# Optimization experiments

Hardware: AMD Instinct MI355X
Metric: run time of the kernel (lower is better)

The kernel has to match this reference:

```python
import jax, jax.numpy as jnp
import numpy as np

WSIZE = (12, 12)
NUM_HEADS = 12
HEAD_DIM = 64


def _rel_idx(ws):
    wh, ww = ws
    num_dist = (2 * wh - 1) * (2 * ww - 1) + 3
    coords = np.stack(np.meshgrid(np.arange(wh), np.arange(ww), indexing='ij'))
    coords = coords.reshape(2, -1)                       # [2, wh*ww]
    rel = (coords[:, :, None] - coords[:, None, :]).transpose(1, 2, 0)
    rel[:, :, 0] += wh - 1
    rel[:, :, 1] += ww - 1
    rel[:, :, 0] *= 2 * ww - 1
    idx = np.zeros((wh * ww + 1,) * 2, dtype=np.int32)
    idx[1:, 1:] = rel.sum(-1)
    idx[0, 0:] = num_dist - 3
    idx[0:, 0] = num_dist - 2
    idx[0, 0] = num_dist - 1
    return idx.flatten()                                  # [(wh*ww+1)**2]

REL_IDX = jnp.asarray(_rel_idx(WSIZE))


def setup_inputs() -> dict:
    key = jax.random.key(0)
    ks = jax.random.split(key, 8)
    B, S, D = 1024, WSIZE[0] * WSIZE[1] + 1, NUM_HEADS * HEAD_DIM
    num_dist = (2 * WSIZE[0] - 1) * (2 * WSIZE[1] - 1) + 3
    return {
        'x': jax.random.normal(ks[0], (B, S, D), jnp.float32),
        'attn_mask': jax.random.normal(ks[1], (B, 1, S, S), jnp.float32),
        'Wq': jax.random.normal(ks[2], (D, D), jnp.float32) * 0.02,
        'bq': jnp.zeros((D,), jnp.float32),
        'Wk': jax.random.normal(ks[3], (D, D), jnp.float32) * 0.02,
        'Wv': jax.random.normal(ks[4], (D, D), jnp.float32) * 0.02,
        'bv': jnp.zeros((D,), jnp.float32),
        'rel_bias_tbl': jax.random.normal(ks[5], (num_dist, NUM_HEADS), jnp.float32) * 0.02,
    }


def reference(x, attn_mask, Wq, bq, Wk, Wv, bv, rel_bias_tbl):
    B, S, _ = x.shape
    H, D = NUM_HEADS, HEAD_DIM

    def heads(e):  # [B,S,H*D] -> [B,H,S,D]
        return e.reshape(B, S, H, D).transpose(0, 2, 1, 3)

    q = heads(x @ Wq + bq)
    k = heads(x @ Wk)            # key has no bias
    v = heads(x @ Wv + bv)

    scores = jnp.einsum('bhqd,bhkd->bhqk', q, k) / np.sqrt(D).astype(x.dtype)
    scores = scores + attn_mask
    # relative position bias: gather [S*S, H] -> [S,S,H] -> [1,H,S,S]
    rel_bias = rel_bias_tbl[REL_IDX].reshape(S, S, H).transpose(2, 0, 1)[None]
    scores = scores + rel_bias

    probs = jax.nn.softmax(scores, axis=-1)
    ctx = jnp.einsum('bhqk,bhkd->bhqd', probs, v)          # [B,H,S,D]
    return ctx.transpose(0, 2, 1, 3).reshape(B, S, H * D)
```

## Files before the change

kernel.cpp:

```cpp
#include <hip/hip_runtime.h>
#include <hip/hip_bf16.h>

typedef __bf16 bf16x8 __attribute__((ext_vector_type(8)));
typedef float f32x4 __attribute__((ext_vector_type(4)));
typedef float f32x4u __attribute__((ext_vector_type(4), aligned(4)));

#define NH 12
#define HD 64
#define SEQ 145
#define SP 160
#define DMODEL 768
#define NTOT 2304
#define BDIM 1024
#define RBS 148

__device__ __forceinline__ ushort f2bf(float f) {
  union { float f; uint u; } a; a.f = f;
  uint u = a.u;
  return (ushort)((u + 0x7FFFu + ((u >> 16) & 1u)) >> 16);
}

__device__ __forceinline__ int relidx(int qi, int ki) {
  if (ki == 0) return (qi == 0) ? 531 : 530;
  if (qi == 0) return 529;
  int q = qi - 1, k = ki - 1;
  int qh = q / 12, qw = q - qh * 12;
  int kh = k / 12, kw = k - kh * 12;
  return (qh - kh + 11) * 23 + (qw - kw + 11);
}

__device__ __forceinline__ void gload_lds16(const ushort* g, ushort* l) {
  __builtin_amdgcn_global_load_lds(
      (const __attribute__((address_space(1))) void*)g,
      (__attribute__((address_space(3))) void*)l, 16, 0, 0);
}

#define VMCNT(n) do { asm volatile("s_waitcnt vmcnt(" #n ")" ::: "memory"); \
                      __builtin_amdgcn_sched_barrier(0); } while (0)

__global__ void prep_w(const float* __restrict__ Wq, const float* __restrict__ Wk,
                       const float* __restrict__ Wv, ushort* __restrict__ Wt) {
  int i = blockIdx.x * 256 + threadIdx.x;
  if (i >= NTOT * DMODEL) return;
  int n = i / DMODEL, k = i - n * DMODEL;
  const float* W = (n < DMODEL) ? Wq : (n < 2 * DMODEL ? Wk : Wv);
  int c = n % DMODEL;
  Wt[i] = f2bf(W[k * DMODEL + c]);
}

__global__ void x2bf(const float* __restrict__ x, ushort* __restrict__ xb) {
  const size_t total = (size_t)BDIM * SEQ * DMODEL;
  size_t i = ((size_t)blockIdx.x * 256 + threadIdx.x) * 8;
  if (i >= total) return;
  float4 a = *reinterpret_cast<const float4*>(x + i);
  float4 c = *reinterpret_cast<const float4*>(x + i + 4);
  uint4 o;
  o.x = (uint)f2bf(a.x) | ((uint)f2bf(a.y) << 16);
  o.y = (uint)f2bf(a.z) | ((uint)f2bf(a.w) << 16);
  o.z = (uint)f2bf(c.x) | ((uint)f2bf(c.y) << 16);
  o.w = (uint)f2bf(c.z) | ((uint)f2bf(c.w) << 16);
  *reinterpret_cast<uint4*>(xb + i) = o;
}

__global__ void zero_vpad(ushort* __restrict__ vbuf) {
  int i = blockIdx.x * 256 + threadIdx.x;
  const int total = BDIM * NH * HD * (SP - SEQ);
  if (i >= total) return;
  int s = SEQ + i % (SP - SEQ);
  int row = i / (SP - SEQ);
  vbuf[(size_t)row * SP + s] = 0;
}

__global__ void rel_prep(const float* __restrict__ tbl, float* __restrict__ rbias) {
  int i = blockIdx.x * 256 + threadIdx.x;
  if (i >= NH * SEQ * RBS) return;
  int h = i / (SEQ * RBS);
  int rem = i - h * SEQ * RBS;
  int qi = rem / RBS, ki = rem - qi * RBS;
  rbias[i] = (ki < SEQ) ? tbl[relidx(qi, ki) * NH + h] : 0.f;
}

#define GNT 9
#define GNWG 10440
#define NKT 24

__global__ __launch_bounds__(512, 4)
void qkv_gemm(const ushort* __restrict__ xb, const ushort* __restrict__ Wt,
              const float* __restrict__ bq, const float* __restrict__ bv,
              ushort* __restrict__ qbuf, ushort* __restrict__ kbuf,
              ushort* __restrict__ vbuf) {
  __shared__ __align__(16) ushort lds[36864];

  int bid = blockIdx.x;
  int logical = (bid & 7) * 1305 + (bid >> 3);
  int mt = logical / GNT, nt = logical - (logical / GNT) * GNT;
  int m0 = mt * 128, n0 = nt * 256;

  int tid = threadIdx.x;
  int l = tid & 63, w = tid >> 6;
  int wm = w >> 2, wn = w & 3;
  int l15 = l & 15, l4 = l >> 4;
  int rslot = l4 ^ ((l15 >> 1) & 3);

  int srow = tid >> 2;
  int schunk = (tid & 3) ^ ((tid >> 3) & 3);
  const ushort* aSrc  = xb + (size_t)(m0 + srow) * DMODEL + schunk * 8;
  const ushort* bSrc0 = Wt + (size_t)(n0 + srow) * DMODEL + schunk * 8;
  const ushort* bSrc1 = Wt + (size_t)(n0 + 128 + srow) * DMODEL + schunk * 8;
  int wdst = w << 9;

#define STAGE(db, kof) do { \
    gload_lds16(aSrc  + (kof), &lds[(db) * 4096 + wdst]); \
    gload_lds16(bSrc0 + (kof), &lds[12288 + (db) * 8192 + wdst]); \
    gload_lds16(bSrc1 + (kof), &lds[12288 + (db) * 8192 + 4096 + wdst]); \
  } while (0)

  f32x4 acc[4][4];
  #pragma unroll
  for (int m = 0; m < 4; m++)
    #pragma unroll
    for (int n = 0; n < 4; n++)
      #pragma unroll
      for (int e = 0; e < 4; e++) acc[m][n][e] = 0.f;

  bf16x8 af[4], bfv[4];

#define LOADFRAG(db) do { \
    int ab_ = (db) * 4096, bb_ = 12288 + (db) * 8192; \
    _Pragma("unroll") \
    for (int i_ = 0; i_ < 4; i_++) \
      af[i_] = *reinterpret_cast<const bf16x8*>( \
          &lds[ab_ + ((wm * 64 + i_ * 16 + l15) << 5) + rslot * 8]); \
    _Pragma("unroll") \
    for (int n_ = 0; n_ < 4; n_++) \
      bfv[n_] = *reinterpret_cast<const bf16x8*>( \
          &lds[bb_ + ((wn * 64 + n_ * 16 + l15) << 5) + rslot * 8]); \
  } while (0)
#define MFMA16() do { \
    __builtin_amdgcn_s_setprio(1); \
    _Pragma("unroll") \
    for (int i_ = 0; i_ < 4; i_++) \
      _Pragma("unroll") \
      for (int n_ = 0; n_ < 4; n_++) \
        acc[i_][n_] = __builtin_amdgcn_mfma_f32_16x16x32_bf16( \
            af[i_], bfv[n_], acc[i_][n_], 0, 0, 0); \
    __builtin_amdgcn_s_setprio(0); \
  } while (0)

  STAGE(0, 0);
  STAGE(1, 32);
  VMCNT(3);
  __builtin_amdgcn_s_barrier();

  #pragma unroll
  for (int t = 0; t < NKT; ++t) {
    int cur = t % 3, nx2 = (t + 2) % 3;
    if (t + 2 < NKT) STAGE(nx2, (t + 2) * 32);
    LOADFRAG(cur);
    MFMA16();
    if (t < NKT - 1) {
      if (t + 2 < NKT) { VMCNT(3); }
      else             { VMCNT(0); }
      __builtin_amdgcn_s_barrier();
    }
  }

  int which = n0 / DMODEL;
  int h_[4], dh_[4];
  float bias_[4];
  #pragma unroll
  for (int nn = 0; nn < 4; nn++) {
    int col = n0 + wn * 64 + nn * 16 + l15;
    int hcol = col - which * DMODEL;
    h_[nn] = hcol >> 6; dh_[nn] = hcol & 63;
    bias_[nn] = (which == 0) ? bq[hcol] : (which == 2 ? bv[hcol] : 0.f);
  }

  if (which != 2) {
    #pragma unroll
    for (int i = 0; i < 4; i++) {
      #pragma unroll
      for (int r = 0; r < 4; r++) {
        int row = m0 + wm * 64 + i * 16 + (l4 << 2) + r;
        int b = row / SEQ;
        int s = row - b * SEQ;
        #pragma unroll
        for (int nn = 0; nn < 4; nn++) {
          float v = acc[i][nn][r] + bias_[nn];
          size_t bh = (size_t)b * NH + h_[nn];
          if (which == 0) {
            v *= 0.125f;
            qbuf[(bh * SEQ + s) * HD + dh_[nn]] = f2bf(v);
          } else {
            kbuf[(bh * SEQ + s) * HD + dh_[nn]] = f2bf(v);
          }
        }
      }
    }
  } else {
    __syncthreads();
    ushort* T = &lds[w * 4608];
    #pragma unroll
    for (int i = 0; i < 4; i++) {
      #pragma unroll
      for (int nn = 0; nn < 4; nn++) {
        int cl = nn * 16 + l15;
        int rl = i * 16 + (l4 << 2);
        ushort4 pk;
        pk.x = f2bf(acc[i][nn][0] + bias_[nn]);
        pk.y = f2bf(acc[i][nn][1] + bias_[nn]);
        pk.z = f2bf(acc[i][nn][2] + bias_[nn]);
        pk.w = f2bf(acc[i][nn][3] + bias_[nn]);
        *reinterpret_cast<ushort4*>(&T[cl * 72 + rl]) = pk;
      }
    }
    asm volatile("s_waitcnt lgkmcnt(0)" ::: "memory");
    __builtin_amdgcn_sched_barrier(0);
    int hU = ((n0 - 2 * DMODEL) >> 6) + wn;
    int rowbase = m0 + wm * 64;
    #pragma unroll
    for (int c = 0; c < 8; c++) {
      uint4 vv = *reinterpret_cast<const uint4*>(&T[l * 72 + c * 8]);
      int R = rowbase + c * 8;
      int b0 = R / SEQ;
      int b7 = (R + 7) / SEQ;
      if (b0 == b7) {
        int s0 = R - b0 * SEQ;
        size_t addr = (((size_t)b0 * NH + hU) * HD + l) * SP + s0;
        *reinterpret_cast<uint4*>(vbuf + addr) = vv;
      } else {
        const ushort* pv = reinterpret_cast<const ushort*>(&vv);
        #pragma unroll
        for (int e = 0; e < 8; e++) {
          int row = R + e;
          int bb = row / SEQ, ss = row - bb * SEQ;
          vbuf[(((size_t)bb * NH + hU) * HD + l) * SP + ss] = pv[e];
        }
      }
    }
  }
#undef STAGE
#undef LOADFRAG
#undef MFMA16
}

#define AH 4
__global__ __launch_bounds__(256, 2)
void attn_kernel(const ushort* __restrict__ qbuf, const ushort* __restrict__ kbuf,
                 const ushort* __restrict__ vbuf, const float* __restrict__ mask,
                 const float* __restrict__ rbias, float* __restrict__ out) {
  __shared__ __align__(16) ushort plds[AH][16][SP + 8];

  int id = blockIdx.x;
  int xcd = id & 7;
  int j = id >> 3;
  int b = xcd + 8 * (j / 30);
  int rem = j % 30;
  int strip = rem / 3, hg = rem % 3;
  int r0 = strip * 16;

  int tid = threadIdx.x;
  int lane = tid & 63, w = tid >> 6;
  int h = hg * AH + w;
  int l15 = lane & 15, l4 = lane >> 4;
  int bh = b * NH + h;

  int qi = r0 + l15;
  int qc = (qi < SEQ) ? qi : (SEQ - 1);
  bool qok = (qi < SEQ);

  const ushort* qp = qbuf + (size_t)bh * SEQ * HD;
  const ushort* kp = kbuf + (size_t)bh * SEQ * HD;
  const ushort* vp = vbuf + (size_t)bh * HD * SP;
  const float* mrow = mask + (size_t)b * SEQ * SEQ + (size_t)qc * SEQ;
  const float* rp = rbias + (size_t)h * SEQ * RBS + (size_t)qc * RBS;

  uint4 qr0, qr1;
  if (qok) {
    qr0 = *reinterpret_cast<const uint4*>(qp + qi * HD + l4 * 8);
    qr1 = *reinterpret_cast<const uint4*>(qp + qi * HD + 32 + l4 * 8);
  } else {
    qr0 = make_uint4(0, 0, 0, 0); qr1 = qr0;
  }
  uint4 kfa[10];
  #pragma unroll
  for (int ct = 0; ct < 5; ct++) {
    int krow = ct * 16 + l15;
    kfa[2 * ct]     = *reinterpret_cast<const uint4*>(kp + krow * HD + l4 * 8);
    kfa[2 * ct + 1] = *reinterpret_cast<const uint4*>(kp + krow * HD + 32 + l4 * 8);
  }
  f32x4 sc[10];
  #pragma unroll
  for (int ct = 0; ct < 5; ct++) {
    int kb = ct * 16 + l4 * 4;
    f32x4u rb = *reinterpret_cast<const f32x4u*>(rp + kb);
    f32x4u mk = *reinterpret_cast<const f32x4u*>(mrow + kb);
    #pragma unroll
    for (int r = 0; r < 4; r++)
      sc[ct][r] = qok ? (mk[r] + rb[r]) : -3e38f;
  }
  uint4 kfb[10];
  #pragma unroll
  for (int ct = 5; ct < 10; ct++) {
    int krow = ct * 16 + l15;
    if (krow >= SEQ) krow = 0;
    kfb[2 * (ct - 5)]     = *reinterpret_cast<const uint4*>(kp + krow * HD + l4 * 8);
    kfb[2 * (ct - 5) + 1] = *reinterpret_cast<const uint4*>(kp + krow * HD + 32 + l4 * 8);
  }
  __builtin_amdgcn_sched_barrier(0);

  bf16x8 qf0 = *reinterpret_cast<bf16x8*>(&qr0);
  bf16x8 qf1 = *reinterpret_cast<bf16x8*>(&qr1);
  #pragma unroll
  for (int ct = 0; ct < 5; ct++) {
    sc[ct] = __builtin_amdgcn_mfma_f32_16x16x32_bf16(
        *reinterpret_cast<bf16x8*>(&kfa[2 * ct]), qf0, sc[ct], 0, 0, 0);
    sc[ct] = __builtin_amdgcn_mfma_f32_16x16x32_bf16(
        *reinterpret_cast<bf16x8*>(&kfa[2 * ct + 1]), qf1, sc[ct], 0, 0, 0);
  }
  #pragma unroll
  for (int ct = 5; ct < 9; ct++) {
    int kb = ct * 16 + l4 * 4;
    f32x4u rb = *reinterpret_cast<const f32x4u*>(rp + kb);
    f32x4u mk = *reinterpret_cast<const f32x4u*>(mrow + kb);
    #pragma unroll
    for (int r = 0; r < 4; r++)
      sc[ct][r] = qok ? (mk[r] + rb[r]) : -3e38f;
  }
  {
    float iv = (l4 == 0 && qok) ? (mrow[144] + rp[144]) : -3e38f;
    sc[9][0] = iv; sc[9][1] = -3e38f; sc[9][2] = -3e38f; sc[9][3] = -3e38f;
  }
  #pragma unroll
  for (int ct = 5; ct < 10; ct++) {
    sc[ct] = __builtin_amdgcn_mfma_f32_16x16x32_bf16(
        *reinterpret_cast<bf16x8*>(&kfb[2 * (ct - 5)]), qf0, sc[ct], 0, 0, 0);
    sc[ct] = __builtin_amdgcn_mfma_f32_16x16x32_bf16(
        *reinterpret_cast<bf16x8*>(&kfb[2 * (ct - 5) + 1]), qf1, sc[ct], 0, 0, 0);
  }
  __builtin_amdgcn_sched_barrier(0);

  uint4 vba[10];
  #pragma unroll
  for (int t = 0; t < 10; t++) {
    int ntl = t / 5, ks = t % 5;
    vba[t] = *reinterpret_cast<const uint4*>(
        vp + (ntl * 16 + l15) * SP + ks * 32 + l4 * 8);
  }
  __builtin_amdgcn_sched_barrier(0);

  float mx = -3e38f;
  #pragma unroll
  for (int ct = 0; ct < 10; ct++)
    #pragma unroll
    for (int r = 0; r < 4; r++) mx = fmaxf(mx, sc[ct][r]);
  mx = fmaxf(mx, __shfl_xor(mx, 16, 64));
  mx = fmaxf(mx, __shfl_xor(mx, 32, 64));
  float sum = 0.f;
  #pragma unroll
  for (int ct = 0; ct < 10; ct++)
    #pragma unroll
    for (int r = 0; r < 4; r++) {
      float p = __expf(sc[ct][r] - mx);
      sc[ct][r] = p;
      sum += p;
    }
  sum += __shfl_xor(sum, 16, 64);
  sum += __shfl_xor(sum, 32, 64);
  float inv = 1.f / sum;

  #pragma unroll
  for (int ct = 0; ct < 10; ct++) {
    ushort4 pk;
    pk.x = f2bf(sc[ct][0] * inv);
    pk.y = f2bf(sc[ct][1] * inv);
    pk.z = f2bf(sc[ct][2] * inv);
    pk.w = f2bf(sc[ct][3] * inv);
    *reinterpret_cast<ushort4*>(&plds[w][l15][ct * 16 + l4 * 4]) = pk;
  }

  uint4 vbb[10];
  #pragma unroll
  for (int t = 0; t < 10; t++) {
    int ntl = 2 + t / 5, ks = t % 5;
    vbb[t] = *reinterpret_cast<const uint4*>(
        vp + (ntl * 16 + l15) * SP + ks * 32 + l4 * 8);
  }
  __builtin_amdgcn_sched_barrier(0);

  #pragma unroll
  for (int ntl = 0; ntl < 2; ntl++) {
    f32x4 pacc;
    #pragma unroll
    for (int e = 0; e < 4; e++) pacc[e] = 0.f;
    #pragma unroll
    for (int ks = 0; ks < 5; ks++) {
      bf16x8 pa = *reinterpret_cast<const bf16x8*>(
          &plds[w][l15][ks * 32 + l4 * 8]);
      pacc = __builtin_amdgcn_mfma_f32_16x16x32_bf16(
          pa, *reinterpret_cast<bf16x8*>(&vba[ntl * 5 + ks]), pacc, 0, 0, 0);
    }
    #pragma unroll
    for (int r = 0; r < 4; r++) {
      int s = r0 + l4 * 4 + r;
      if (s < SEQ)
        out[((size_t)b * SEQ + s) * DMODEL + h * HD + ntl * 16 + l15] = pacc[r];
    }
  }
  #pragma unroll
  for (int ntl = 2; ntl < 4; ntl++) {
    f32x4 pacc;
    #pragma unroll
    for (int e = 0; e < 4; e++) pacc[e] = 0.f;
    #pragma unroll
    for (int ks = 0; ks < 5; ks++) {
      bf16x8 pa = *reinterpret_cast<const bf16x8*>(
          &plds[w][l15][ks * 32 + l4 * 8]);
      pacc = __builtin_amdgcn_mfma_f32_16x16x32_bf16(
          pa, *reinterpret_cast<bf16x8*>(&vbb[(ntl - 2) * 5 + ks]), pacc, 0, 0, 0);
    }
    #pragma unroll
    for (int r = 0; r < 4; r++) {
      int s = r0 + l4 * 4 + r;
      if (s < SEQ)
        out[((size_t)b * SEQ + s) * DMODEL + h * HD + ntl * 16 + l15] = pacc[r];
    }
  }
}

extern "C" void kernel_launch(void* const* d_in, const int* in_sizes, int n_in,
                              void* d_out, int out_size, void* d_ws, size_t ws_size,
                              hipStream_t stream) {
  const float* x    = (const float*)d_in[0];
  const float* mask = (const float*)d_in[1];
  const float* Wq   = (const float*)d_in[2];
  const float* bq   = (const float*)d_in[3];
  const float* Wk   = (const float*)d_in[4];
  const float* Wv   = (const float*)d_in[5];
  const float* bv   = (const float*)d_in[6];
  const float* tbl  = (const float*)d_in[7];
  float* out = (float*)d_out;

  char* ws = (char*)d_ws;
  ushort* Wt = (ushort*)ws;
  size_t off = (size_t)NTOT * DMODEL * 2;
  ushort* qbuf = (ushort*)(ws + off); off += (size_t)BDIM * NH * SEQ * HD * 2;
  ushort* kbuf = (ushort*)(ws + off); off += (size_t)BDIM * NH * SEQ * HD * 2;
  ushort* vbuf = (ushort*)(ws + off); off += (size_t)BDIM * NH * HD * SP * 2;
  float*  rbias = (float*)(ws + off); off += (size_t)NH * SEQ * RBS * 4 + 64;

  ushort* xbuf = (ushort*)d_out;

  prep_w<<<(NTOT * DMODEL + 255) / 256, 256, 0, stream>>>(Wq, Wk, Wv, Wt);
  zero_vpad<<<(BDIM * NH * HD * (SP - SEQ) + 255) / 256, 256, 0, stream>>>(vbuf);
  rel_prep<<<(NH * SEQ * RBS + 255) / 256, 256, 0, stream>>>(tbl, rbias);
  {
    size_t total = (size_t)BDIM * SEQ * DMODEL;
    x2bf<<<(int)(total / 8 / 256), 256, 0, stream>>>(x, xbuf);
  }

  qkv_gemm<<<GNWG, 512, 0, stream>>>(xbuf, Wt, bq, bv, qbuf, kbuf, vbuf);

  attn_kernel<<<BDIM * 10 * 3, 256, 0, stream>>>(qbuf, kbuf, vbuf, mask, rbias, out);
}
```

Before: 1.438 ms.

## Loop over query strips per block, keeping K and V in registers

Each attention block used to handle one 16-row query strip, so K and V for a (batch, head) were reloaded from global memory by ten separate blocks. Now each block loops over all ten strips and keeps the K and V fragments in registers across the loop, so they are loaded once. The grid shrinks tenfold to 3072 blocks. In exchange, register pressure rises (40 uint4 fragments held across the loop), there is less parallelism, and the strip loop runs serially, which reduces the latency hiding that came from interleaving loads with MFMAs.

```diff
diff --git a/kernel.cpp b/kernel.cpp
--- a/kernel.cpp
+++ b/kernel.cpp
@@ -254,10 +254,8 @@
   int id = blockIdx.x;
   int xcd = id & 7;
   int j = id >> 3;
-  int b = xcd + 8 * (j / 30);
-  int rem = j % 30;
-  int strip = rem / 3, hg = rem % 3;
-  int r0 = strip * 16;
+  int b = xcd + 8 * (j / 3);
+  int hg = j % 3;
 
   int tid = threadIdx.x;
   int lane = tid & 63, w = tid >> 6;
@@ -265,41 +263,19 @@
   int l15 = lane & 15, l4 = lane >> 4;
   int bh = b * NH + h;
 
-  int qi = r0 + l15;
-  int qc = (qi < SEQ) ? qi : (SEQ - 1);
-  bool qok = (qi < SEQ);
-
   const ushort* qp = qbuf + (size_t)bh * SEQ * HD;
   const ushort* kp = kbuf + (size_t)bh * SEQ * HD;
   const ushort* vp = vbuf + (size_t)bh * HD * SP;
-  const float* mrow = mask + (size_t)b * SEQ * SEQ + (size_t)qc * SEQ;
-  const float* rp = rbias + (size_t)h * SEQ * RBS + (size_t)qc * RBS;
-
-  uint4 qr0, qr1;
-  if (qok) {
-    qr0 = *reinterpret_cast<const uint4*>(qp + qi * HD + l4 * 8);
-    qr1 = *reinterpret_cast<const uint4*>(qp + qi * HD + 32 + l4 * 8);
-  } else {
-    qr0 = make_uint4(0, 0, 0, 0); qr1 = qr0;
-  }
-  uint4 kfa[10];
+  const float* mbase = mask + (size_t)b * SEQ * SEQ;
+  const float* rbase = rbias + (size_t)h * SEQ * RBS;
+
+  uint4 kfa[10], kfb[10];
   #pragma unroll
   for (int ct = 0; ct < 5; ct++) {
     int krow = ct * 16 + l15;
     kfa[2 * ct]     = *reinterpret_cast<const uint4*>(kp + krow * HD + l4 * 8);
     kfa[2 * ct + 1] = *reinterpret_cast<const uint4*>(kp + krow * HD + 32 + l4 * 8);
   }
-  f32x4 sc[10];
-  #pragma unroll
-  for (int ct = 0; ct < 5; ct++) {
-    int kb = ct * 16 + l4 * 4;
-    f32x4u rb = *reinterpret_cast<const f32x4u*>(rp + kb);
-    f32x4u mk = *reinterpret_cast<const f32x4u*>(mrow + kb);
-    #pragma unroll
-    for (int r = 0; r < 4; r++)
-      sc[ct][r] = qok ? (mk[r] + rb[r]) : -3e38f;
-  }
-  uint4 kfb[10];
   #pragma unroll
   for (int ct = 5; ct < 10; ct++) {
     int krow = ct * 16 + l15;
@@ -307,123 +283,136 @@
     kfb[2 * (ct - 5)]     = *reinterpret_cast<const uint4*>(kp + krow * HD + l4 * 8);
     kfb[2 * (ct - 5) + 1] = *reinterpret_cast<const uint4*>(kp + krow * HD + 32 + l4 * 8);
   }
-  __builtin_amdgcn_sched_barrier(0);
-
-  bf16x8 qf0 = *reinterpret_cast<bf16x8*>(&qr0);
-  bf16x8 qf1 = *reinterpret_cast<bf16x8*>(&qr1);
-  #pragma unroll
-  for (int ct = 0; ct < 5; ct++) {
-    sc[ct] = __builtin_amdgcn_mfma_f32_16x16x32_bf16(
-        *reinterpret_cast<bf16x8*>(&kfa[2 * ct]), qf0, sc[ct], 0, 0, 0);
-    sc[ct] = __builtin_amdgcn_mfma_f32_16x16x32_bf16(
-        *reinterpret_cast<bf16x8*>(&kfa[2 * ct + 1]), qf1, sc[ct], 0, 0, 0);
-  }
-  #pragma unroll
-  for (int ct = 5; ct < 9; ct++) {
-    int kb = ct * 16 + l4 * 4;
-    f32x4u rb = *reinterpret_cast<const f32x4u*>(rp + kb);
-    f32x4u mk = *reinterpret_cast<const f32x4u*>(mrow + kb);
-    #pragma unroll
-    for (int r = 0; r < 4; r++)
-      sc[ct][r] = qok ? (mk[r] + rb[r]) : -3e38f;
-  }
-  {
-    float iv = (l4 == 0 && qok) ? (mrow[144] + rp[144]) : -3e38f;
-    sc[9][0] = iv; sc[9][1] = -3e38f; sc[9][2] = -3e38f; sc[9][3] = -3e38f;
-  }
-  #pragma unroll
-  for (int ct = 5; ct < 10; ct++) {
-    sc[ct] = __builtin_amdgcn_mfma_f32_16x16x32_bf16(
-        *reinterpret_cast<bf16x8*>(&kfb[2 * (ct - 5)]), qf0, sc[ct], 0, 0, 0);
-    sc[ct] = __builtin_amdgcn_mfma_f32_16x16x32_bf16(
-        *reinterpret_cast<bf16x8*>(&kfb[2 * (ct - 5) + 1]), qf1, sc[ct], 0, 0, 0);
-  }
-  __builtin_amdgcn_sched_barrier(0);
-
-  uint4 vba[10];
+  uint4 vba[10], vbb[10];
   #pragma unroll
   for (int t = 0; t < 10; t++) {
     int ntl = t / 5, ks = t % 5;
     vba[t] = *reinterpret_cast<const uint4*>(
         vp + (ntl * 16 + l15) * SP + ks * 32 + l4 * 8);
   }
-  __builtin_amdgcn_sched_barrier(0);
-
-  float mx = -3e38f;
-  #pragma unroll
-  for (int ct = 0; ct < 10; ct++)
-    #pragma unroll
-    for (int r = 0; r < 4; r++) mx = fmaxf(mx, sc[ct][r]);
-  mx = fmaxf(mx, __shfl_xor(mx, 16, 64));
-  mx = fmaxf(mx, __shfl_xor(mx, 32, 64));
-  float sum = 0.f;
-  #pragma unroll
-  for (int ct = 0; ct < 10; ct++)
-    #pragma unroll
-    for (int r = 0; r < 4; r++) {
-      float p = __expf(sc[ct][r] - mx);
-      sc[ct][r] = p;
-      sum += p;
-    }
-  sum += __shfl_xor(sum, 16, 64);
-  sum += __shfl_xor(sum, 32, 64);
-  float inv = 1.f / sum;
-
-  #pragma unroll
-  for (int ct = 0; ct < 10; ct++) {
-    ushort4 pk;
-    pk.x = f2bf(sc[ct][0] * inv);
-    pk.y = f2bf(sc[ct][1] * inv);
-    pk.z = f2bf(sc[ct][2] * inv);
-    pk.w = f2bf(sc[ct][3] * inv);
-    *reinterpret_cast<ushort4*>(&plds[w][l15][ct * 16 + l4 * 4]) = pk;
-  }
-
-  uint4 vbb[10];
   #pragma unroll
   for (int t = 0; t < 10; t++) {
     int ntl = 2 + t / 5, ks = t % 5;
     vbb[t] = *reinterpret_cast<const uint4*>(
         vp + (ntl * 16 + l15) * SP + ks * 32 + l4 * 8);
   }
-  __builtin_amdgcn_sched_barrier(0);
-
-  #pragma unroll
-  for (int ntl = 0; ntl < 2; ntl++) {
-    f32x4 pacc;
-    #pragma unroll
-    for (int e = 0; e < 4; e++) pacc[e] = 0.f;
-    #pragma unroll
-    for (int ks = 0; ks < 5; ks++) {
-      bf16x8 pa = *reinterpret_cast<const bf16x8*>(
-          &plds[w][l15][ks * 32 + l4 * 8]);
-      pacc = __builtin_amdgcn_mfma_f32_16x16x32_bf16(
-          pa, *reinterpret_cast<bf16x8*>(&vba[ntl * 5 + ks]), pacc, 0, 0, 0);
-    }
-    #pragma unroll
-    for (int r = 0; r < 4; r++) {
-      int s = r0 + l4 * 4 + r;
-      if (s < SEQ)
-        out[((size_t)b * SEQ + s) * DMODEL + h * HD + ntl * 16 + l15] = pacc[r];
-    }
-  }
-  #pragma unroll
-  for (int ntl = 2; ntl < 4; ntl++) {
-    f32x4 pacc;
-    #pragma unroll
-    for (int e = 0; e < 4; e++) pacc[e] = 0.f;
-    #pragma unroll
-    for (int ks = 0; ks < 5; ks++) {
-      bf16x8 pa = *reinterpret_cast<const bf16x8*>(
-          &plds[w][l15][ks * 32 + l4 * 8]);
-      pacc = __builtin_amdgcn_mfma_f32_16x16x32_bf16(
-          pa, *reinterpret_cast<bf16x8*>(&vbb[(ntl - 2) * 5 + ks]), pacc, 0, 0, 0);
-    }
-    #pragma unroll
-    for (int r = 0; r < 4; r++) {
-      int s = r0 + l4 * 4 + r;
-      if (s < SEQ)
-        out[((size_t)b * SEQ + s) * DMODEL + h * HD + ntl * 16 + l15] = pacc[r];
+
+  #pragma unroll 1
+  for (int strip = 0; strip < 10; strip++) {
+    int r0 = strip * 16;
+    int qi = r0 + l15;
+    int qc = (qi < SEQ) ? qi : (SEQ - 1);
+    bool qok = (qi < SEQ);
+    const float* mrow = mbase + (size_t)qc * SEQ;
+    const float* rp = rbase + (size_t)qc * RBS;
+
+    bf16x8 qf0, qf1;
+    if (qok) {
+      qf0 = *reinterpret_cast<const bf16x8*>(qp + qi * HD + l4 * 8);
+      qf1 = *reinterpret_cast<const bf16x8*>(qp + qi * HD + 32 + l4 * 8);
+    } else {
+      uint4 z = make_uint4(0, 0, 0, 0);
+      qf0 = *reinterpret_cast<bf16x8*>(&z);
+      qf1 = *reinterpret_cast<bf16x8*>(&z);
+    }
+
+    f32x4 sc[10];
+    #pragma unroll
+    for (int ct = 0; ct < 9; ct++) {
+      int kb = ct * 16 + l4 * 4;
+      f32x4u rb = *reinterpret_cast<const f32x4u*>(rp + kb);
+      f32x4u mk = *reinterpret_cast<const f32x4u*>(mrow + kb);
+      #pragma unroll
+      for (int r = 0; r < 4; r++)
+        sc[ct][r] = qok ? (mk[r] + rb[r]) : -3e38f;
+    }
+    {
+      float iv = (l4 == 0 && qok) ? (mrow[144] + rp[144]) : -3e38f;
+      sc[9][0] = iv; sc[9][1] = -3e38f; sc[9][2] = -3e38f; sc[9][3] = -3e38f;
+    }
+
+    #pragma unroll
+    for (int ct = 0; ct < 5; ct++) {
+      sc[ct] = __builtin_amdgcn_mfma_f32_16x16x32_bf16(
+          *reinterpret_cast<bf16x8*>(&kfa[2 * ct]), qf0, sc[ct], 0, 0, 0);
+      sc[ct] = __builtin_amdgcn_mfma_f32_16x16x32_bf16(
+          *reinterpret_cast<bf16x8*>(&kfa[2 * ct + 1]), qf1, sc[ct], 0, 0, 0);
+    }
+    #pragma unroll
+    for (int ct = 5; ct < 10; ct++) {
+      sc[ct] = __builtin_amdgcn_mfma_f32_16x16x32_bf16(
+          *reinterpret_cast<bf16x8*>(&kfb[2 * (ct - 5)]), qf0, sc[ct], 0, 0, 0);
+      sc[ct] = __builtin_amdgcn_mfma_f32_16x16x32_bf16(
+          *reinterpret_cast<bf16x8*>(&kfb[2 * (ct - 5) + 1]), qf1, sc[ct], 0, 0, 0);
+    }
+
+    float mx = -3e38f;
+    #pragma unroll
+    for (int ct = 0; ct < 10; ct++)
+      #pragma unroll
+      for (int r = 0; r < 4; r++) mx = fmaxf(mx, sc[ct][r]);
+    mx = fmaxf(mx, __shfl_xor(mx, 16, 64));
+    mx = fmaxf(mx, __shfl_xor(mx, 32, 64));
+    float sum = 0.f;
+    #pragma unroll
+    for (int ct = 0; ct < 10; ct++)
+      #pragma unroll
+      for (int r = 0; r < 4; r++) {
+        float p = __expf(sc[ct][r] - mx);
+        sc[ct][r] = p;
+        sum += p;
+      }
+    sum += __shfl_xor(sum, 16, 64);
+    sum += __shfl_xor(sum, 32, 64);
+    float inv = 1.f / sum;
+
+    #pragma unroll
+    for (int ct = 0; ct < 10; ct++) {
+      ushort4 pk;
+      pk.x = f2bf(sc[ct][0] * inv);
+      pk.y = f2bf(sc[ct][1] * inv);
+      pk.z = f2bf(sc[ct][2] * inv);
+      pk.w = f2bf(sc[ct][3] * inv);
+      *reinterpret_cast<ushort4*>(&plds[w][l15][ct * 16 + l4 * 4]) = pk;
+    }
+
+    #pragma unroll
+    for (int ntl = 0; ntl < 2; ntl++) {
+      f32x4 pacc;
+      #pragma unroll
+      for (int e = 0; e < 4; e++) pacc[e] = 0.f;
+      #pragma unroll
+      for (int ks = 0; ks < 5; ks++) {
+        bf16x8 pa = *reinterpret_cast<const bf16x8*>(
+            &plds[w][l15][ks * 32 + l4 * 8]);
+        pacc = __builtin_amdgcn_mfma_f32_16x16x32_bf16(
+            pa, *reinterpret_cast<bf16x8*>(&vba[ntl * 5 + ks]), pacc, 0, 0, 0);
+      }
+      #pragma unroll
+      for (int r = 0; r < 4; r++) {
+        int s = r0 + l4 * 4 + r;
+        if (s < SEQ)
+          out[((size_t)b * SEQ + s) * DMODEL + h * HD + ntl * 16 + l15] = pacc[r];
+      }
+    }
+    #pragma unroll
+    for (int ntl = 2; ntl < 4; ntl++) {
+      f32x4 pacc;
+      #pragma unroll
+      for (int e = 0; e < 4; e++) pacc[e] = 0.f;
+      #pragma unroll
+      for (int ks = 0; ks < 5; ks++) {
+        bf16x8 pa = *reinterpret_cast<const bf16x8*>(
+            &plds[w][l15][ks * 32 + l4 * 8]);
+        pacc = __builtin_amdgcn_mfma_f32_16x16x32_bf16(
+            pa, *reinterpret_cast<bf16x8*>(&vbb[(ntl - 2) * 5 + ks]), pacc, 0, 0, 0);
+      }
+      #pragma unroll
+      for (int r = 0; r < 4; r++) {
+        int s = r0 + l4 * 4 + r;
+        if (s < SEQ)
+          out[((size_t)b * SEQ + s) * DMODEL + h * HD + ntl * 16 + l15] = pacc[r];
+      }
     }
   }
 }
@@ -461,5 +450,5 @@
 
   qkv_gemm<<<GNWG, 512, 0, stream>>>(xbuf, Wt, bq, bv, qbuf, kbuf, vbuf);
 
-  attn_kernel<<<BDIM * 10 * 3, 256, 0, stream>>>(qbuf, kbuf, vbuf, mask, rbias, out);
-}
+  attn_kernel<<<BDIM * 3, 256, 0, stream>>>(qbuf, kbuf, vbuf, mask, rbias, out);
+}
```

New measurement: 1.231 ms (median of 2 runs). -14.4%, faster.
